# Performance work log

Hardware: AMD Instinct MI355X
Metric: run time of the kernel (lower is better)

## Reference

```python
import jax, jax.numpy as jnp
import numpy as np

T, B, E, H = 512, 128, 512, 512
MEM, CTX = 500, 300

def setup_inputs() -> dict:
    key = jax.random.key(0)
    ks = jax.random.split(key, 16)
    s = 0.05
    return {
        "input_seqs": jax.random.normal(ks[0], (B, T, E), jnp.float32),
        "input_lengths": jax.random.randint(ks[1], (B,), 1, T + 1),
        "Wih_f": jax.random.normal(ks[2], (4 * H, E + CTX), jnp.float32) * s,
        "Whh_f": jax.random.normal(ks[3], (4 * H, H), jnp.float32) * s,
        "bih_f": jax.random.normal(ks[4], (4 * H,), jnp.float32) * s,
        "bhh_f": jax.random.normal(ks[5], (4 * H,), jnp.float32) * s,
        "Wih_b": jax.random.normal(ks[6], (4 * H, E + CTX), jnp.float32) * s,
        "Whh_b": jax.random.normal(ks[7], (4 * H, H), jnp.float32) * s,
        "bih_b": jax.random.normal(ks[8], (4 * H,), jnp.float32) * s,
        "bhh_b": jax.random.normal(ks[9], (4 * H,), jnp.float32) * s,
        "Mk_f": jax.random.normal(ks[10], (MEM, H), jnp.float32) * s,
        "Mv_f": jax.random.normal(ks[11], (CTX, MEM), jnp.float32) * s,
        "Mk_b": jax.random.normal(ks[12], (MEM, H), jnp.float32) * s,
        "Mv_b": jax.random.normal(ks[13], (CTX, MEM), jnp.float32) * s,
    }

def _mem_ctx(h, Mk, Mv):
    # exp-key softmax read: exp(h Mk^T) normalized by row sum, then project to CTX
    a = jnp.exp(h @ Mk.T)                      # [B, MEM]
    return (a / jnp.sum(a, axis=-1, keepdims=True)) @ Mv.T  # [B, CTX]

def _cell(x, h, c, Wih, Whh, b):
    g = x @ Wih.T + h @ Whh.T + b              # [B, 4H], gate order i,f,g,o
    i, f, gg, o = jnp.split(g, 4, axis=-1)
    c = jax.nn.sigmoid(f) * c + jax.nn.sigmoid(i) * jnp.tanh(gg)
    return jax.nn.sigmoid(o) * jnp.tanh(c), c

def reference(input_seqs, input_lengths, Wih_f, Whh_f, bih_f, bhh_f,
              Wih_b, Whh_b, bih_b, bhh_b, Mk_f, Mv_f, Mk_b, Mv_b):
    xs = jnp.transpose(input_seqs, (1, 0, 2))          # [T, B, E]
    dt = xs.dtype
    mask = (jnp.arange(T)[:, None] < input_lengths[None, :]).astype(dt)[:, :, None]  # [T,B,1]
    b_f = bih_f + bhh_f
    b_b = bih_b + bhh_b
    z = jnp.zeros((B, H), dt)
    zf = jnp.zeros((), dt)
    one = jnp.ones((), dt)

    def fstep(carry, x):
        h, c, flag = carry
        ctx = flag * _mem_ctx(h, Mk_f, Mv_f)           # step 0 uses zero dummy context
        h, c = _cell(jnp.concatenate([x, ctx], -1), h, c, Wih_f, Whh_f, b_f)
        return (h, c, one), h
    _, f_hs = jax.lax.scan(fstep, (z, z, zf), xs)      # [T, B, H] per-step hidden

    def bstep(carry, xm):
        x, m = xm
        hm, h, c, flag = carry
        ctx = flag * _mem_ctx(hm, Mk_b, Mv_b)
        h, c = _cell(jnp.concatenate([x, ctx], -1), h, c, Wih_b, Whh_b, b_b)
        return (h * m, h, c, one), None                # masked hidden feeds next memory read
    (h_b, _, _, _), _ = jax.lax.scan(bstep, (z, z, z, zf), (xs[::-1], mask[::-1]))

    idx = jnp.clip(input_lengths - 1, 0, T - 1)
    h_f = f_hs[idx, jnp.arange(B)]                     # final valid forward hidden per example
    # permute(1,2,0).view(B,-1): interleave fwd/bwd per hidden unit
    return jnp.stack([h_f, h_b], axis=-1).reshape(B, 2 * H)
```

## Files before the change

kernel.cpp:

```cpp
#include <hip/hip_runtime.h>
#include <hip/hip_bf16.h>

#define T_   512
#define B_   128
#define E_   512
#define H_   512
#define G4_  2048
#define MEM_ 500
#define CTX_ 300
#define EC_  (E_ + CTX_)
#define SPIN_MAX 65536

typedef short sh8  __attribute__((ext_vector_type(8)));
typedef float f32x4 __attribute__((ext_vector_type(4)));

struct ScanParams {
  const float* __restrict__ x;
  const short* __restrict__ xbf;
  const int*   __restrict__ len;
  const float* __restrict__ Wih0; const float* __restrict__ Whh0;
  const float* __restrict__ bih0; const float* __restrict__ bhh0;
  const float* __restrict__ Wih1; const float* __restrict__ Whh1;
  const float* __restrict__ bih1; const float* __restrict__ bhh1;
  const float* __restrict__ Mk0;  const float* __restrict__ Mk1;
  const float* __restrict__ Mf;
  short* __restrict__ hbf;
  short* __restrict__ hmbf;
  short* __restrict__ aB;
  unsigned* __restrict__ bar;
  float* __restrict__ out;
};

__device__ __forceinline__ float sigm_(float x) { return 1.f / (1.f + __expf(-x)); }
__device__ __forceinline__ float tanh_(float x) { return 1.f - 2.f / (__expf(2.f * x) + 1.f); }
__device__ __forceinline__ short f2bs(float f) {
  __hip_bfloat16 h = __float2bfloat16(f);
  short s; __builtin_memcpy(&s, &h, 2); return s;
}
__device__ __forceinline__ float bs2f(short s) {
  unsigned u = ((unsigned)(unsigned short)s) << 16;
  float f; __builtin_memcpy(&f, &u, 4); return f;
}

struct F16 { sh8 v[16]; };
__device__ __forceinline__ void gld16(F16& f, const short* base) {
  asm volatile(
      "global_load_dwordx4 %0, %16, off sc1\n\t"
      "global_load_dwordx4 %1, %16, off offset:64 sc1\n\t"
      "global_load_dwordx4 %2, %16, off offset:128 sc1\n\t"
      "global_load_dwordx4 %3, %16, off offset:192 sc1\n\t"
      "global_load_dwordx4 %4, %16, off offset:256 sc1\n\t"
      "global_load_dwordx4 %5, %16, off offset:320 sc1\n\t"
      "global_load_dwordx4 %6, %16, off offset:384 sc1\n\t"
      "global_load_dwordx4 %7, %16, off offset:448 sc1\n\t"
      "global_load_dwordx4 %8, %16, off offset:512 sc1\n\t"
      "global_load_dwordx4 %9, %16, off offset:576 sc1\n\t"
      "global_load_dwordx4 %10, %16, off offset:640 sc1\n\t"
      "global_load_dwordx4 %11, %16, off offset:704 sc1\n\t"
      "global_load_dwordx4 %12, %16, off offset:768 sc1\n\t"
      "global_load_dwordx4 %13, %16, off offset:832 sc1\n\t"
      "global_load_dwordx4 %14, %16, off offset:896 sc1\n\t"
      "global_load_dwordx4 %15, %16, off offset:960 sc1\n\t"
      "s_waitcnt vmcnt(0)"
      : "=&v"(f.v[0]), "=&v"(f.v[1]), "=&v"(f.v[2]), "=&v"(f.v[3]),
        "=&v"(f.v[4]), "=&v"(f.v[5]), "=&v"(f.v[6]), "=&v"(f.v[7]),
        "=&v"(f.v[8]), "=&v"(f.v[9]), "=&v"(f.v[10]), "=&v"(f.v[11]),
        "=&v"(f.v[12]), "=&v"(f.v[13]), "=&v"(f.v[14]), "=&v"(f.v[15])
      : "v"(base)
      : "memory");
}

__device__ __forceinline__ void st4s(short* base, unsigned d0, unsigned d1,
                                     unsigned d2, unsigned d3) {
  asm volatile(
      "global_store_short %4, %0, off sc1\n\t"
      "global_store_short %4, %1, off offset:1024 sc1\n\t"
      "global_store_short %4, %2, off offset:2048 sc1\n\t"
      "global_store_short %4, %3, off offset:3072 sc1\n\t"
      "s_waitcnt vmcnt(0)"
      :: "v"(d0), "v"(d1), "v"(d2), "v"(d3), "v"(base) : "memory");
}

__device__ __forceinline__ void st8s(short* base, const unsigned* d) {
  asm volatile(
      "global_store_short %8, %0, off sc1\n\t"
      "global_store_short %8, %1, off offset:1024 sc1\n\t"
      "global_store_short %8, %2, off offset:2048 sc1\n\t"
      "global_store_short %8, %3, off offset:3072 sc1\n\t"
      "global_store_short %8, %4, off offset:8 sc1\n\t"
      "global_store_short %8, %5, off offset:1032 sc1\n\t"
      "global_store_short %8, %6, off offset:2056 sc1\n\t"
      "global_store_short %8, %7, off offset:3080 sc1"
      :: "v"(d[0]), "v"(d[1]), "v"(d[2]), "v"(d[3]),
         "v"(d[4]), "v"(d[5]), "v"(d[6]), "v"(d[7]), "v"(base) : "memory");
}

__device__ __forceinline__ bool hchk(const unsigned* hfl, int wv, unsigned ep, int lane) {
  unsigned v = __hip_atomic_load(&hfl[((lane * 8) + wv) * 16],
                                 __ATOMIC_RELAXED, __HIP_MEMORY_SCOPE_AGENT);
  return __all((int)(v >= ep));
}
__device__ __forceinline__ bool achk(const unsigned* afl, int wv, unsigned ep, int lane) {
  unsigned v = __hip_atomic_load(&afl[(((lane & 31) * 8) + wv) * 16],
                                 __ATOMIC_RELAXED, __HIP_MEMORY_SCOPE_AGENT);
  return __all((int)(v >= ep));
}
__device__ __forceinline__ void spin_h(const unsigned* hfl, int wv, unsigned ep, int lane) {
  int n = 0;
  while (!hchk(hfl, wv, ep, lane) && n < SPIN_MAX) { __builtin_amdgcn_s_sleep(1); ++n; }
}
__device__ __forceinline__ void spin_a(const unsigned* afl, int wv, unsigned ep, int lane) {
  int n = 0;
  while (!achk(afl, wv, ep, lane) && n < SPIN_MAX) { __builtin_amdgcn_s_sleep(1); ++n; }
}
__device__ __forceinline__ void fset(unsigned* slot, unsigned ep, int lane) {
  if (lane == 0)
    __hip_atomic_store(slot, ep, __ATOMIC_RELAXED, __HIP_MEMORY_SCOPE_AGENT);
}

__global__ __launch_bounds__(256) void xcvt_kernel(const float* __restrict__ x,
                                                   short* __restrict__ xbf) {
  const size_t i = ((size_t)blockIdx.x * 256 + threadIdx.x) * 8;
  f32x4 a = *reinterpret_cast<const f32x4*>(x + i);
  f32x4 b = *reinterpret_cast<const f32x4*>(x + i + 4);
  sh8 v;
  #pragma unroll
  for (int j = 0; j < 4; ++j) { v[j] = f2bs(a[j]); v[4 + j] = f2bs(b[j]); }
  *reinterpret_cast<sh8*>(xbf + i) = v;
}

__global__ __launch_bounds__(256) void mfused_kernel(
    const float* __restrict__ WihF, const float* __restrict__ WihB,
    const float* __restrict__ MvF,  const float* __restrict__ MvB,
    float* __restrict__ Mf) {
  const int d  = blockIdx.x >> 7;
  const int j0 = (blockIdx.x & 127) * 16;
  const float* __restrict__ Wih = d ? WihB : WihF;
  const float* __restrict__ Mv  = d ? MvB  : MvF;
  __shared__ float Wl[16][CTX_ + 1];
  for (int i = threadIdx.x; i < 16 * CTX_; i += 256) {
    int r = i / CTX_, cc = i - r * CTX_;
    Wl[r][cc] = Wih[(size_t)(j0 + r) * EC_ + E_ + cc];
  }
  __syncthreads();
  const int jj = threadIdx.x & 15;
  for (int m = threadIdx.x >> 4; m < MEM_; m += 16) {
    float acc = 0.f;
    for (int cc = 0; cc < CTX_; ++cc)
      acc = fmaf(Mv[cc * MEM_ + m], Wl[jj][cc], acc);
    Mf[(size_t)d * MEM_ * G4_ + (size_t)m * G4_ + j0 + jj] = acc;
  }
}

__global__ __launch_bounds__(512, 1) void scan_kernel(ScanParams p) {
  const int dir  = blockIdx.x >> 6;
  const int w    = blockIdx.x & 63;
  const int tid  = threadIdx.x;
  const int wv   = tid >> 6;
  const int lane = tid & 63;

  __shared__ __align__(16) short WgL[32 * 2 * 64 * 8];
  __shared__ __align__(16) short MkL[16 * 64 * 8];
  __shared__ __align__(16) short MfL[16 * 2 * 64 * 8];
  __shared__ int LvL[B_];

  const float* __restrict__ Wihd = dir ? p.Wih1 : p.Wih0;
  const float* __restrict__ Whhd = dir ? p.Whh1 : p.Whh0;
  const float* __restrict__ bihd = dir ? p.bih1 : p.bih0;
  const float* __restrict__ bhhd = dir ? p.bhh1 : p.bhh0;
  const float* __restrict__ Mkd  = dir ? p.Mk1  : p.Mk0;
  const float* __restrict__ Mfd  = p.Mf + (size_t)dir * MEM_ * G4_;
  short* __restrict__ aBd = p.aB + (size_t)dir * B_ * 512;

  unsigned* __restrict__ hflD = p.bar + (size_t)dir * 64 * 8 * 16;
  unsigned* __restrict__ aflD = p.bar + 16384 + (size_t)dir * 32 * 8 * 16;

  const bool prod = ((w & 1) == dir);
  const int  ct   = w >> 1;

  for (int i = tid; i < 32 * 2 * 64; i += 512) {
    const int ks = i >> 7, r2 = i & 127, ct2 = r2 >> 6, l2 = r2 & 63;
    const int col = l2 & 15, kg = l2 >> 4;
    const int k0 = ks * 32 + kg * 8;
    const int gc = (col & 3) * H_ + 8 * w + 4 * ct2 + (col >> 2);
    const float* src = (k0 < E_) ? (Wihd + (size_t)gc * EC_ + k0)
                                 : (Whhd + (size_t)gc * H_ + (k0 - E_));
    sh8 v;
    #pragma unroll
    for (int j = 0; j < 8; ++j) v[j] = f2bs(src[j]);
    *reinterpret_cast<sh8*>(&WgL[i * 8]) = v;
  }
  for (int i = tid; i < 16 * 64; i += 512) {
    const int ks = i >> 6, l2 = i & 63;
    const int col = l2 & 15, kg = l2 >> 4;
    const int k0 = ks * 32 + kg * 8;
    const int mr = 16 * ct + col;
    sh8 v;
    #pragma unroll
    for (int j = 0; j < 8; ++j)
      v[j] = (mr < MEM_) ? f2bs(Mkd[(size_t)mr * H_ + k0 + j]) : (short)0;
    *reinterpret_cast<sh8*>(&MkL[i * 8]) = v;
  }
  for (int i = tid; i < 16 * 2 * 64; i += 512) {
    const int ks = i >> 7, r2 = i & 127, ct2 = r2 >> 6, l2 = r2 & 63;
    const int col = l2 & 15, kg = l2 >> 4;
    const int gc = (col & 3) * H_ + 8 * w + 4 * ct2 + (col >> 2);
    const int m0 = ks * 32 + kg * 8;
    sh8 v;
    #pragma unroll
    for (int j = 0; j < 8; ++j)
      v[j] = (m0 + j < MEM_) ? f2bs(Mfd[(size_t)(m0 + j) * G4_ + gc]) : (short)0;
    *reinterpret_cast<sh8*>(&MfL[i * 8]) = v;
  }
  if (tid < B_) LvL[tid] = p.len[tid];

  const int cc  = lane & 15;
  const int q   = cc & 3;
  const int uu  = cc >> 2;
  const int kg8 = (lane >> 4) * 8;
  const int arow = lane & 15;
  float biasl[2];
  #pragma unroll
  for (int ct2 = 0; ct2 < 2; ++ct2) {
    const int gc = q * H_ + 8 * w + 4 * ct2 + uu;
    biasl[ct2] = bihd[gc] + bhhd[gc];
  }

  float creg[2][4] = {{0.f,0.f,0.f,0.f},{0.f,0.f,0.f,0.f}};
  __syncthreads();

  auto xhalf = [&](int t, f32x4* acc) {
    if (p.xbf) {
      const short* xb = p.xbf + ((size_t)(16 * wv + arow) * T_ + t) * E_ + kg8;
      for (int ks = 0; ks < 16; ++ks) {
        sh8 af = *reinterpret_cast<const sh8*>(xb + ks * 32);
        acc[0] = __builtin_amdgcn_mfma_f32_16x16x32_bf16(
            af, *reinterpret_cast<const sh8*>(&WgL[((ks * 2 + 0) * 64 + lane) * 8]), acc[0], 0, 0, 0);
        acc[1] = __builtin_amdgcn_mfma_f32_16x16x32_bf16(
            af, *reinterpret_cast<const sh8*>(&WgL[((ks * 2 + 1) * 64 + lane) * 8]), acc[1], 0, 0, 0);
      }
    } else {
      const float* xp0 = p.x + ((size_t)(16 * wv + arow) * T_ + t) * E_ + kg8;
      for (int ks = 0; ks < 16; ++ks) {
        f32x4 v0 = *reinterpret_cast<const f32x4*>(xp0 + ks * 32);
        f32x4 v1 = *reinterpret_cast<const f32x4*>(xp0 + ks * 32 + 4);
        sh8 af;
        #pragma unroll
        for (int j = 0; j < 4; ++j) { af[j] = f2bs(v0[j]); af[4 + j] = f2bs(v1[j]); }
        acc[0] = __builtin_amdgcn_mfma_f32_16x16x32_bf16(
            af, *reinterpret_cast<const sh8*>(&WgL[((ks * 2 + 0) * 64 + lane) * 8]), acc[0], 0, 0, 0);
        acc[1] = __builtin_amdgcn_mfma_f32_16x16x32_bf16(
            af, *reinterpret_cast<const sh8*>(&WgL[((ks * 2 + 1) * 64 + lane) * 8]), acc[1], 0, 0, 0);
      }
    }
  };

  f32x4 accG[2] = {(f32x4){0,0,0,0}, (f32x4){0,0,0,0}};
  xhalf(dir ? T_ - 1 : 0, accG);

  const bool bwdprod = prod && dir;

  for (int s = 0; s < T_; ++s) {
    const int t   = dir ? (T_ - 1 - s) : s;
    const int cur = s & 1, prv = cur ^ 1;
    const short* __restrict__ hb_prev = p.hbf + ((size_t)(prv * 2 + dir)) * B_ * H_;
    short*       __restrict__ hb_cur  = p.hbf + ((size_t)(cur * 2 + dir)) * B_ * H_;
    const short* __restrict__ hm_prev = p.hmbf + (size_t)prv * B_ * H_;
    short*       __restrict__ hm_cur  = p.hmbf + (size_t)cur * B_ * H_;

    const short* hrow = hb_prev + (size_t)(16 * wv + arow) * H_ + kg8;
    const short* mrow = hm_prev + (size_t)(16 * wv + arow) * H_ + kg8;

    if (s > 0) spin_h(hflD, wv, (unsigned)s, lane);
    __builtin_amdgcn_sched_barrier(0);
    F16 fH, fM;
    gld16(fH, hrow);
    if (bwdprod) gld16(fM, mrow);

    if (prod) {
      f32x4 accA = (f32x4){0, 0, 0, 0};
      if (dir) {
        for (int ks = 0; ks < 16; ++ks)
          accA = __builtin_amdgcn_mfma_f32_16x16x32_bf16(
              fM.v[ks], *reinterpret_cast<const sh8*>(&MkL[(ks * 64 + lane) * 8]), accA, 0, 0, 0);
      } else {
        for (int ks = 0; ks < 16; ++ks)
          accA = __builtin_amdgcn_mfma_f32_16x16x32_bf16(
              fH.v[ks], *reinterpret_cast<const sh8*>(&MkL[(ks * 64 + lane) * 8]), accA, 0, 0, 0);
      }
      const int m = 16 * ct + arow;
      unsigned d[4];
      #pragma unroll
      for (int r = 0; r < 4; ++r) {
        float e = (m < MEM_) ? __expf(accA[r]) : 0.f;
        d[r] = (unsigned)(unsigned short)f2bs(e);
      }
      st4s(aBd + (size_t)(16 * wv + 4 * (lane >> 4)) * 512 + m, d[0], d[1], d[2], d[3]);
      fset(&aflD[(ct * 8 + wv) * 16], (unsigned)(s + 1), lane);
    }

    for (int ks = 0; ks < 16; ++ks) {
      accG[0] = __builtin_amdgcn_mfma_f32_16x16x32_bf16(
          fH.v[ks], *reinterpret_cast<const sh8*>(&WgL[(((16 + ks) * 2 + 0) * 64 + lane) * 8]), accG[0], 0, 0, 0);
      accG[1] = __builtin_amdgcn_mfma_f32_16x16x32_bf16(
          fH.v[ks], *reinterpret_cast<const sh8*>(&WgL[(((16 + ks) * 2 + 1) * 64 + lane) * 8]), accG[1], 0, 0, 0);
    }

    f32x4 accC[2] = {(f32x4){0,0,0,0}, (f32x4){0,0,0,0}};
    float inv4[4] = {0.f, 0.f, 0.f, 0.f};
    if (s > 0) {
      spin_a(aflD, wv, (unsigned)(s + 1), lane);
      __builtin_amdgcn_sched_barrier(0);
      F16 fC;
      gld16(fC, aBd + (size_t)(16 * wv + arow) * 512 + kg8);
      float rs = 0.f;
      for (int ks = 0; ks < 16; ++ks) {
        accC[0] = __builtin_amdgcn_mfma_f32_16x16x32_bf16(
            fC.v[ks], *reinterpret_cast<const sh8*>(&MfL[((ks * 2 + 0) * 64 + lane) * 8]), accC[0], 0, 0, 0);
        accC[1] = __builtin_amdgcn_mfma_f32_16x16x32_bf16(
            fC.v[ks], *reinterpret_cast<const sh8*>(&MfL[((ks * 2 + 1) * 64 + lane) * 8]), accC[1], 0, 0, 0);
        #pragma unroll
        for (int j = 0; j < 8; ++j) rs += bs2f(fC.v[ks][j]);
      }
      rs += __shfl_xor(rs, 16);
      rs += __shfl_xor(rs, 32);
      #pragma unroll
      for (int r = 0; r < 4; ++r)
        inv4[r] = 1.f / __shfl(rs, 4 * (lane >> 4) + r);
    }

    unsigned hsd[8]; unsigned hmd[8]; float hvv[2][4];
    #pragma unroll
    for (int ct2 = 0; ct2 < 2; ++ct2) {
      float g4[4];
      #pragma unroll
      for (int r = 0; r < 4; ++r) {
        float v = accG[ct2][r] + biasl[ct2];
        if (s > 0) v += accC[ct2][r] * inv4[r];
        g4[r] = v;
      }
      #pragma unroll
      for (int r = 0; r < 4; ++r) {
        const float x1 = __shfl_xor(g4[r], 1);
        const float x2 = __shfl_xor(g4[r], 2);
        const float x3 = __shfl_xor(g4[r], 3);
        const float iv = (q==0)?g4[r]:(q==1)?x1:(q==2)?x2:x3;
        const float fv = (q==0)?x1:(q==1)?g4[r]:(q==2)?x3:x2;
        const float gv = (q==0)?x2:(q==1)?x3:(q==2)?g4[r]:x1;
        const float ov = (q==0)?x3:(q==1)?x2:(q==2)?x1:g4[r];
        float cv = creg[ct2][r];
        cv = sigm_(fv) * cv + sigm_(iv) * tanh_(gv);
        const float hv = sigm_(ov) * tanh_(cv);
        creg[ct2][r] = cv;
        hvv[ct2][r] = hv;
        const short hs = f2bs(hv);
        hsd[ct2 * 4 + r] = (unsigned)(unsigned short)hs;
        if (dir) {
          const int b = 16 * wv + 4 * (lane >> 4) + r;
          hmd[ct2 * 4 + r] = (t < LvL[b]) ? hsd[ct2 * 4 + r] : 0u;
        }
      }
    }
    if (q == 0) {
      const int b0 = 16 * wv + 4 * (lane >> 4);
      const int unit0 = 8 * w + uu;
      unsigned hord[8] = {hsd[0],hsd[1],hsd[2],hsd[3],hsd[4],hsd[5],hsd[6],hsd[7]};
      st8s(hb_cur + (size_t)b0 * H_ + unit0, hord);
      if (dir) {
        unsigned mord[8] = {hmd[0],hmd[1],hmd[2],hmd[3],hmd[4],hmd[5],hmd[6],hmd[7]};
        st8s(hm_cur + (size_t)b0 * H_ + unit0, mord);
      }
      #pragma unroll
      for (int ct2 = 0; ct2 < 2; ++ct2) {
        #pragma unroll
        for (int r = 0; r < 4; ++r) {
          const int b = b0 + r;
          const int unit = unit0 + 4 * ct2;
          if (dir == 0) {
            if (t == LvL[b] - 1) p.out[b * (2 * H_) + 2 * unit] = hvv[ct2][r];
          } else {
            if (s == T_ - 1) p.out[b * (2 * H_) + 2 * unit + 1] = hvv[ct2][r];
          }
        }
      }
    }
    asm volatile("s_waitcnt vmcnt(0)" ::: "memory");
    fset(&hflD[(w * 8 + wv) * 16], (unsigned)(s + 1), lane);

    accG[0] = (f32x4){0,0,0,0}; accG[1] = (f32x4){0,0,0,0};
    if (s + 1 < T_) xhalf(dir ? (T_ - 2 - s) : (s + 1), accG);
  }
}

extern "C" void kernel_launch(void* const* d_in, const int* in_sizes, int n_in,
                              void* d_out, int out_size, void* d_ws, size_t ws_size,
                              hipStream_t stream) {
  (void)in_sizes; (void)n_in; (void)out_size;

  ScanParams p;
  p.x    = (const float*)d_in[0];
  p.len  = (const int*)  d_in[1];
  p.Wih0 = (const float*)d_in[2];
  p.Whh0 = (const float*)d_in[3];
  p.bih0 = (const float*)d_in[4];
  p.bhh0 = (const float*)d_in[5];
  p.Wih1 = (const float*)d_in[6];
  p.Whh1 = (const float*)d_in[7];
  p.bih1 = (const float*)d_in[8];
  p.bhh1 = (const float*)d_in[9];
  p.Mk0  = (const float*)d_in[10];
  const float* MvF = (const float*)d_in[11];
  p.Mk1  = (const float*)d_in[12];
  const float* MvB = (const float*)d_in[13];

  char* ws = (char*)d_ws;
  size_t off = 0;
  auto alloc = [&](size_t bytes) -> void* {
    void* ptr = ws + off; off += (bytes + 255) & ~(size_t)255; return ptr;
  };
  float*    Mf   = (float*)   alloc((size_t)2 * MEM_ * G4_ * 4);
  short*    hbf  = (short*)   alloc((size_t)2 * 2 * B_ * H_ * 2);
  short*    hmbf = (short*)   alloc((size_t)2 * B_ * H_ * 2);
  short*    aB   = (short*)   alloc((size_t)2 * B_ * 512 * 2);
  unsigned* bar  = (unsigned*)alloc((size_t)24576 * sizeof(unsigned));
  size_t xbf_off = off;
  short*    xbf  = (short*)   alloc((size_t)B_ * T_ * E_ * 2);
  const bool useXbf = (ws_size >= xbf_off + (size_t)B_ * T_ * E_ * 2);

  p.Mf = Mf; p.hbf = hbf; p.hmbf = hmbf; p.aB = aB; p.bar = bar;
  p.xbf = useXbf ? xbf : nullptr;
  p.out = (float*)d_out;

  hipMemsetAsync(hbf, 0, (size_t)(2 * 2 + 2) * B_ * H_ * 2, stream);
  hipMemsetAsync(bar, 0, (size_t)24576 * sizeof(unsigned), stream);

  if (useXbf) {
    const size_t n8 = (size_t)B_ * T_ * E_ / 8;
    xcvt_kernel<<<dim3((unsigned)(n8 / 256)), dim3(256), 0, stream>>>(p.x, xbf);
  }
  mfused_kernel<<<dim3(256), dim3(256), 0, stream>>>(
      (const float*)d_in[2], (const float*)d_in[6], MvF, MvB, Mf);

  void* args[] = { &p };
  hipLaunchCooperativeKernel((const void*)scan_kernel, dim3(128), dim3(512),
                             args, 0, stream);
}
```

Before: 9.656 ms.

## Compact barrier flags, derive masked hidden in-register, overlap next-step input GEMM

Packs the per-wave readiness flags into contiguous arrays, one per wave and direction, so a spin check reads adjacent words instead of 64-byte-strided slots. Drops the separate masked-hidden buffer in the backward direction: the producer zeroes the loaded hidden fragment when the step is past the sequence length, which removes a second gather and a second store per step. Moves the next step's input-projection MFMAs to just before the memory-context wait, so they can overlap that wait instead of running after the flag is set. Packing flags tightly may add cache-line contention between writers, and the zeroing relies on mask equivalence at t+1 < len.

```diff
diff --git a/kernel.cpp b/kernel.cpp
--- a/kernel.cpp
+++ b/kernel.cpp
@@ -25,7 +25,6 @@
   const float* __restrict__ Mk0;  const float* __restrict__ Mk1;
   const float* __restrict__ Mf;
   short* __restrict__ hbf;
-  short* __restrict__ hmbf;
   short* __restrict__ aB;
   unsigned* __restrict__ bar;
   float* __restrict__ out;
@@ -95,23 +94,21 @@
          "v"(d[4]), "v"(d[5]), "v"(d[6]), "v"(d[7]), "v"(base) : "memory");
 }
 
-__device__ __forceinline__ bool hchk(const unsigned* hfl, int wv, unsigned ep, int lane) {
-  unsigned v = __hip_atomic_load(&hfl[((lane * 8) + wv) * 16],
-                                 __ATOMIC_RELAXED, __HIP_MEMORY_SCOPE_AGENT);
+__device__ __forceinline__ bool hchk(const unsigned* hflW, unsigned ep, int lane) {
+  unsigned v = __hip_atomic_load(&hflW[lane], __ATOMIC_RELAXED, __HIP_MEMORY_SCOPE_AGENT);
   return __all((int)(v >= ep));
 }
-__device__ __forceinline__ bool achk(const unsigned* afl, int wv, unsigned ep, int lane) {
-  unsigned v = __hip_atomic_load(&afl[(((lane & 31) * 8) + wv) * 16],
-                                 __ATOMIC_RELAXED, __HIP_MEMORY_SCOPE_AGENT);
+__device__ __forceinline__ bool achk(const unsigned* aflW, unsigned ep, int lane) {
+  unsigned v = __hip_atomic_load(&aflW[lane & 31], __ATOMIC_RELAXED, __HIP_MEMORY_SCOPE_AGENT);
   return __all((int)(v >= ep));
 }
-__device__ __forceinline__ void spin_h(const unsigned* hfl, int wv, unsigned ep, int lane) {
+__device__ __forceinline__ void spin_h(const unsigned* hflW, unsigned ep, int lane) {
   int n = 0;
-  while (!hchk(hfl, wv, ep, lane) && n < SPIN_MAX) { __builtin_amdgcn_s_sleep(1); ++n; }
-}
-__device__ __forceinline__ void spin_a(const unsigned* afl, int wv, unsigned ep, int lane) {
+  while (!hchk(hflW, ep, lane) && n < SPIN_MAX) { __builtin_amdgcn_s_sleep(1); ++n; }
+}
+__device__ __forceinline__ void spin_a(const unsigned* aflW, unsigned ep, int lane) {
   int n = 0;
-  while (!achk(afl, wv, ep, lane) && n < SPIN_MAX) { __builtin_amdgcn_s_sleep(1); ++n; }
+  while (!achk(aflW, ep, lane) && n < SPIN_MAX) { __builtin_amdgcn_s_sleep(1); ++n; }
 }
 __device__ __forceinline__ void fset(unsigned* slot, unsigned ep, int lane) {
   if (lane == 0)
@@ -172,8 +169,8 @@
   const float* __restrict__ Mfd  = p.Mf + (size_t)dir * MEM_ * G4_;
   short* __restrict__ aBd = p.aB + (size_t)dir * B_ * 512;
 
-  unsigned* __restrict__ hflD = p.bar + (size_t)dir * 64 * 8 * 16;
-  unsigned* __restrict__ aflD = p.bar + 16384 + (size_t)dir * 32 * 8 * 16;
+  unsigned* __restrict__ hflW = p.bar + (size_t)(dir * 8 + wv) * 64;
+  unsigned* __restrict__ aflW = p.bar + 1024 + (size_t)(dir * 8 + wv) * 32;
 
   const bool prod = ((w & 1) == dir);
   const int  ct   = w >> 1;
@@ -228,6 +225,8 @@
 
   float creg[2][4] = {{0.f,0.f,0.f,0.f},{0.f,0.f,0.f,0.f}};
   __syncthreads();
+
+  const int mylen = LvL[16 * wv + arow];
 
   auto xhalf = [&](int t, f32x4* acc) {
     if (p.xbf) {
@@ -255,34 +254,34 @@
     }
   };
 
-  f32x4 accG[2] = {(f32x4){0,0,0,0}, (f32x4){0,0,0,0}};
-  xhalf(dir ? T_ - 1 : 0, accG);
-
-  const bool bwdprod = prod && dir;
+  f32x4 accX[2] = {(f32x4){0,0,0,0}, (f32x4){0,0,0,0}};
+  xhalf(dir ? T_ - 1 : 0, accX);
 
   for (int s = 0; s < T_; ++s) {
     const int t   = dir ? (T_ - 1 - s) : s;
     const int cur = s & 1, prv = cur ^ 1;
     const short* __restrict__ hb_prev = p.hbf + ((size_t)(prv * 2 + dir)) * B_ * H_;
     short*       __restrict__ hb_cur  = p.hbf + ((size_t)(cur * 2 + dir)) * B_ * H_;
-    const short* __restrict__ hm_prev = p.hmbf + (size_t)prv * B_ * H_;
-    short*       __restrict__ hm_cur  = p.hmbf + (size_t)cur * B_ * H_;
 
     const short* hrow = hb_prev + (size_t)(16 * wv + arow) * H_ + kg8;
-    const short* mrow = hm_prev + (size_t)(16 * wv + arow) * H_ + kg8;
-
-    if (s > 0) spin_h(hflD, wv, (unsigned)s, lane);
+
+    f32x4 accG[2] = { accX[0], accX[1] };
+
+    if (s > 0) spin_h(hflW, (unsigned)s, lane);
     __builtin_amdgcn_sched_barrier(0);
-    F16 fH, fM;
+    F16 fH;
     gld16(fH, hrow);
-    if (bwdprod) gld16(fM, mrow);
 
     if (prod) {
       f32x4 accA = (f32x4){0, 0, 0, 0};
       if (dir) {
-        for (int ks = 0; ks < 16; ++ks)
+        const sh8 z8 = (sh8){0,0,0,0,0,0,0,0};
+        const bool keep = (t + 1) < mylen;
+        for (int ks = 0; ks < 16; ++ks) {
+          sh8 af = keep ? fH.v[ks] : z8;
           accA = __builtin_amdgcn_mfma_f32_16x16x32_bf16(
-              fM.v[ks], *reinterpret_cast<const sh8*>(&MkL[(ks * 64 + lane) * 8]), accA, 0, 0, 0);
+              af, *reinterpret_cast<const sh8*>(&MkL[(ks * 64 + lane) * 8]), accA, 0, 0, 0);
+        }
       } else {
         for (int ks = 0; ks < 16; ++ks)
           accA = __builtin_amdgcn_mfma_f32_16x16x32_bf16(
@@ -296,7 +295,7 @@
         d[r] = (unsigned)(unsigned short)f2bs(e);
       }
       st4s(aBd + (size_t)(16 * wv + 4 * (lane >> 4)) * 512 + m, d[0], d[1], d[2], d[3]);
-      fset(&aflD[(ct * 8 + wv) * 16], (unsigned)(s + 1), lane);
+      fset(&aflW[ct], (unsigned)(s + 1), lane);
     }
 
     for (int ks = 0; ks < 16; ++ks) {
@@ -306,10 +305,13 @@
           fH.v[ks], *reinterpret_cast<const sh8*>(&WgL[(((16 + ks) * 2 + 1) * 64 + lane) * 8]), accG[1], 0, 0, 0);
     }
 
+    accX[0] = (f32x4){0,0,0,0}; accX[1] = (f32x4){0,0,0,0};
+    if (s + 1 < T_) xhalf(dir ? (T_ - 2 - s) : (s + 1), accX);
+
     f32x4 accC[2] = {(f32x4){0,0,0,0}, (f32x4){0,0,0,0}};
     float inv4[4] = {0.f, 0.f, 0.f, 0.f};
     if (s > 0) {
-      spin_a(aflD, wv, (unsigned)(s + 1), lane);
+      spin_a(aflW, (unsigned)(s + 1), lane);
       __builtin_amdgcn_sched_barrier(0);
       F16 fC;
       gld16(fC, aBd + (size_t)(16 * wv + arow) * 512 + kg8);
@@ -329,7 +331,7 @@
         inv4[r] = 1.f / __shfl(rs, 4 * (lane >> 4) + r);
     }
 
-    unsigned hsd[8]; unsigned hmd[8]; float hvv[2][4];
+    unsigned hsd[8]; float hvv[2][4];
     #pragma unroll
     for (int ct2 = 0; ct2 < 2; ++ct2) {
       float g4[4];
@@ -353,12 +355,7 @@
         const float hv = sigm_(ov) * tanh_(cv);
         creg[ct2][r] = cv;
         hvv[ct2][r] = hv;
-        const short hs = f2bs(hv);
-        hsd[ct2 * 4 + r] = (unsigned)(unsigned short)hs;
-        if (dir) {
-          const int b = 16 * wv + 4 * (lane >> 4) + r;
-          hmd[ct2 * 4 + r] = (t < LvL[b]) ? hsd[ct2 * 4 + r] : 0u;
-        }
+        hsd[ct2 * 4 + r] = (unsigned)(unsigned short)f2bs(hv);
       }
     }
     if (q == 0) {
@@ -366,10 +363,6 @@
       const int unit0 = 8 * w + uu;
       unsigned hord[8] = {hsd[0],hsd[1],hsd[2],hsd[3],hsd[4],hsd[5],hsd[6],hsd[7]};
       st8s(hb_cur + (size_t)b0 * H_ + unit0, hord);
-      if (dir) {
-        unsigned mord[8] = {hmd[0],hmd[1],hmd[2],hmd[3],hmd[4],hmd[5],hmd[6],hmd[7]};
-        st8s(hm_cur + (size_t)b0 * H_ + unit0, mord);
-      }
       #pragma unroll
       for (int ct2 = 0; ct2 < 2; ++ct2) {
         #pragma unroll
@@ -385,10 +378,7 @@
       }
     }
     asm volatile("s_waitcnt vmcnt(0)" ::: "memory");
-    fset(&hflD[(w * 8 + wv) * 16], (unsigned)(s + 1), lane);
-
-    accG[0] = (f32x4){0,0,0,0}; accG[1] = (f32x4){0,0,0,0};
-    if (s + 1 < T_) xhalf(dir ? (T_ - 2 - s) : (s + 1), accG);
+    fset(&hflW[w], (unsigned)(s + 1), lane);
   }
 }
 
@@ -420,19 +410,18 @@
   };
   float*    Mf   = (float*)   alloc((size_t)2 * MEM_ * G4_ * 4);
   short*    hbf  = (short*)   alloc((size_t)2 * 2 * B_ * H_ * 2);
-  short*    hmbf = (short*)   alloc((size_t)2 * B_ * H_ * 2);
   short*    aB   = (short*)   alloc((size_t)2 * B_ * 512 * 2);
-  unsigned* bar  = (unsigned*)alloc((size_t)24576 * sizeof(unsigned));
+  unsigned* bar  = (unsigned*)alloc((size_t)1536 * sizeof(unsigned));
   size_t xbf_off = off;
   short*    xbf  = (short*)   alloc((size_t)B_ * T_ * E_ * 2);
   const bool useXbf = (ws_size >= xbf_off + (size_t)B_ * T_ * E_ * 2);
 
-  p.Mf = Mf; p.hbf = hbf; p.hmbf = hmbf; p.aB = aB; p.bar = bar;
+  p.Mf = Mf; p.hbf = hbf; p.aB = aB; p.bar = bar;
   p.xbf = useXbf ? xbf : nullptr;
   p.out = (float*)d_out;
 
-  hipMemsetAsync(hbf, 0, (size_t)(2 * 2 + 2) * B_ * H_ * 2, stream);
-  hipMemsetAsync(bar, 0, (size_t)24576 * sizeof(unsigned), stream);
+  hipMemsetAsync(hbf, 0, (size_t)2 * 2 * B_ * H_ * 2, stream);
+  hipMemsetAsync(bar, 0, (size_t)1536 * sizeof(unsigned), stream);
 
   if (useXbf) {
     const size_t n8 = (size_t)B_ * T_ * E_ / 8;
```

New measurement: 9.811 ms. About the same (+1.6%).
